# Optimization experiments

Hardware: AMD Instinct MI355X
Metric: run time of the kernel (lower is better)

The kernel has to match this reference:

```python
import jax, jax.numpy as jnp
import numpy as np

EPS = 1e-5

def _offset_conv(x, w, b):
    # 3x3 conv, padding=1, producing 2*K*K offset channels (standard DeformConv2D v1)
    out = jax.lax.conv_general_dilated(x, w, (1, 1), ((1, 1), (1, 1)),
                                       dimension_numbers=('NCHW', 'OIHW', 'NCHW'))
    return out + b[None, :, None, None]

def _bilinear_gather(x, py, px):
    # x: [B,C,H,W]; py,px: [B,K2,H,W] float sample coords -> [B,C,K2,H,W]
    B, C, H, W = x.shape
    py = jnp.clip(py, 0.0, H - 1.0)
    px = jnp.clip(px, 0.0, W - 1.0)
    y0 = jnp.floor(py)
    x0 = jnp.floor(px)
    wy = py - y0
    wx = px - x0
    y0i = y0.astype(jnp.int32)
    x0i = x0.astype(jnp.int32)
    y1i = jnp.minimum(y0i + 1, H - 1)
    x1i = jnp.minimum(x0i + 1, W - 1)
    xf = x.reshape(B, C, H * W)
    K2, Ho, Wo = py.shape[1], py.shape[2], py.shape[3]
    def gather(yy, xx):
        idx = (yy * W + xx).reshape(B, 1, -1)  # broadcast over C
        return jnp.take_along_axis(xf, idx, axis=2).reshape(B, C, K2, Ho, Wo)
    v00 = gather(y0i, x0i)
    v01 = gather(y0i, x1i)
    v10 = gather(y1i, x0i)
    v11 = gather(y1i, x1i)
    wy = wy[:, None]
    wx = wx[:, None]
    return (v00 * (1 - wy) * (1 - wx) + v01 * (1 - wy) * wx
            + v10 * wy * (1 - wx) + v11 * wy * wx)

def _deform_dw(x, w_off, b_off, w_dw, k):
    # depthwise deformable conv, kernel k, padding k//2 (same spatial size)
    B, C, H, W = x.shape
    K2 = k * k
    off = _offset_conv(x, w_off, b_off)      # [B, 2*K2, H, W]
    dy, dx = off[:, :K2], off[:, K2:]
    r = (k - 1) // 2
    pn = jnp.arange(-r, r + 1, dtype=x.dtype)
    pn_y = jnp.repeat(pn, k)[None, :, None, None]  # [1,K2,1,1]
    pn_x = jnp.tile(pn, k)[None, :, None, None]
    gy = jnp.arange(H, dtype=x.dtype)[None, None, :, None]
    gx = jnp.arange(W, dtype=x.dtype)[None, None, None, :]
    py = gy + pn_y + dy
    px = gx + pn_x + dx
    samp = _bilinear_gather(x, py, px)        # [B,C,K2,H,W]
    return jnp.einsum('bckhw,ck->bchw', samp, w_dw.reshape(C, K2))

def _bn_relu(x, g, b, m, v):
    inv = g / jnp.sqrt(v + EPS)
    return jax.nn.relu(x * inv[None, :, None, None] + (b - m * inv)[None, :, None, None])

def setup_inputs() -> dict:
    key = jax.random.key(0)
    B, C, H, W, O = 4, 96, 64, 64, 192
    ks = jax.random.split(key, 32)
    d = {'x': jax.random.normal(ks[0], (B, C, H, W), jnp.float32)}
    i = 1
    for k in (3, 5, 7):
        K2 = k * k
        d[f'w_off{k}'] = 0.01 * jax.random.normal(ks[i], (2 * K2, C, 3, 3), jnp.float32); i += 1
        d[f'b_off{k}'] = jnp.zeros((2 * K2,), jnp.float32)
        d[f'w_dw{k}'] = jax.random.normal(ks[i], (C, k, k), jnp.float32) / k; i += 1
        d[f'g{k}'] = jnp.ones((C,), jnp.float32)
        d[f'be{k}'] = jnp.zeros((C,), jnp.float32)
        d[f'm{k}'] = 0.1 * jax.random.normal(ks[i], (C,), jnp.float32); i += 1
        d[f'v{k}'] = jax.random.uniform(ks[i], (C,), jnp.float32, 0.5, 1.5); i += 1
    d['w_pw'] = jax.random.normal(ks[i], (O, 3 * C), jnp.float32) / np.sqrt(3 * C).astype(np.float32); i += 1
    d['gp'] = jnp.ones((O,), jnp.float32)
    d['bp'] = jnp.zeros((O,), jnp.float32)
    d['mp'] = 0.1 * jax.random.normal(ks[i], (O,), jnp.float32); i += 1
    d['vp'] = jax.random.uniform(ks[i], (O,), jnp.float32, 0.5, 1.5)
    return d

def reference(x, w_off3, b_off3, w_dw3, g3, be3, m3, v3,
              w_off5, b_off5, w_dw5, g5, be5, m5, v5,
              w_off7, b_off7, w_dw7, g7, be7, m7, v7,
              w_pw, gp, bp, mp, vp):
    x1 = _bn_relu(_deform_dw(x, w_off3, b_off3, w_dw3, 3), g3, be3, m3, v3)
    x2 = _bn_relu(_deform_dw(x, w_off5, b_off5, w_dw5, 5), g5, be5, m5, v5)
    x3 = _bn_relu(_deform_dw(x, w_off7, b_off7, w_dw7, 7), g7, be7, m7, v7)
    xc = jnp.concatenate([x1, x2, x3], axis=1)  # [B, 3C, H, W]
    out = jnp.einsum('bchw,oc->bohw', xc, w_pw)  # 1x1 conv
    return _bn_relu(out, gp, bp, mp, vp)
```

## Files before the change

kernel.cpp:

```cpp
#include <hip/hip_runtime.h>
#include <hip/hip_fp16.h>
#include <math.h>

typedef unsigned short u16;
typedef _Float16 f16x8 __attribute__((ext_vector_type(8)));
typedef float f32x4 __attribute__((ext_vector_type(4)));

#define HWp 4096
#define Cc 96
#define Bb 4
#define Oo 192
#define C3 288

#define OFF_WDWT  0
#define OFF_BCAT  14112
#define OFF_SBR   14304
#define OFF_HBR   14592
#define OFF_SPW   14880
#define OFF_HPW   15072
#define FP32_END  15264
#define BF_XTPAD  0
#define BF_WOF    1672704
#define BF_WPW    1838592

__device__ __forceinline__ u16 f2h(float f) { return __half_as_ushort(__float2half(f)); }
__device__ __forceinline__ unsigned h2u(__half2 h) { union { __half2 h; unsigned u; } t; t.h = h; return t.u; }
__device__ __forceinline__ __half2 u2h(unsigned u) { union { __half2 h; unsigned u; } t; t.u = u; return t.h; }

#define PREP_N (165888 + 55296 + 14112 + 192 + 288 + 288 + 192 + 192 + 24960)
#define PREP_BLK ((PREP_N + 255) / 256)

__global__ __launch_bounds__(256) void prep_kernel(
    const float* __restrict__ x,
    const float* __restrict__ w3, const float* __restrict__ b3, const float* __restrict__ dw3,
    const float* __restrict__ g3, const float* __restrict__ be3, const float* __restrict__ m3, const float* __restrict__ v3,
    const float* __restrict__ w5, const float* __restrict__ b5, const float* __restrict__ dw5,
    const float* __restrict__ g5, const float* __restrict__ be5, const float* __restrict__ m5, const float* __restrict__ v5,
    const float* __restrict__ w7, const float* __restrict__ b7, const float* __restrict__ dw7,
    const float* __restrict__ g7, const float* __restrict__ be7, const float* __restrict__ m7, const float* __restrict__ v7,
    const float* __restrict__ wpw,
    const float* __restrict__ gp, const float* __restrict__ bp, const float* __restrict__ mp, const float* __restrict__ vp,
    float* __restrict__ ws)
{
    __shared__ u16 sT[64 * 104];
    u16* bf = (u16*)(ws + FP32_END);
    const int tid = threadIdx.x;

    if (blockIdx.x < 256) {
        const int b = blockIdx.x >> 6, h = blockIdx.x & 63;
        const float* xb = x + (((size_t)b * Cc) << 12) + (h << 6);
#pragma unroll
        for (int it = 0; it < 24; ++it) {
            int j = tid + it * 256;
            int c = j >> 6, p = j & 63;
            sT[p * 104 + c] = f2h(xb[((size_t)c << 12) + p]);
        }
        __syncthreads();
        u16* dst = bf + BF_XTPAD + ((size_t)(b * 66 + h + 1) * 66 + 1) * 96;
#pragma unroll
        for (int it = 0; it < 6; ++it) {
            int j = tid + it * 256;
            int pos = j / 24, c4 = j % 24;
            const u16* s = &sT[pos * 104 + c4 * 4];
            *(uint2*)(dst + pos * 96 + c4 * 4) = make_uint2(
                (unsigned)s[0] | ((unsigned)s[1] << 16),
                (unsigned)s[2] | ((unsigned)s[3] << 16));
        }
        return;
    }

    int i = (blockIdx.x - 256) * 256 + tid;
    if (i < 165888) {
        int f = i / 13824, r = i % 13824;
        int s = r >> 9, l = r & 511;
        int lane = l >> 3, j = l & 7;
        int o = f * 16 + (lane & 15);
        int k = s * 32 + (lane >> 4) * 8 + j;
        int tap = k / 96, c = k % 96;
        float v = 0.f;
        if (o < 18)       v = w3[o * 864 + c * 9 + tap];
        else if (o < 68)  v = w5[(o - 18) * 864 + c * 9 + tap];
        else if (o < 166) v = w7[(o - 68) * 864 + c * 9 + tap];
        bf[BF_WOF + i] = f2h(v);
        return;
    }
    int j = i - 165888;
    if (j < 55296) {
        int f = j / 4608, r = j % 4608;
        int s = r >> 9, l = r & 511;
        int lane = l >> 3, jj = l & 7;
        int o = f * 16 + (lane & 15);
        int k = s * 32 + (lane >> 4) * 8 + jj;
        bf[BF_WPW + j] = f2h(wpw[o * C3 + k]);
        return;
    }
    j -= 55296;
    if (j < 14112) {
        int ksel = j / 4704, rem = j % 4704;
        int t = rem / 96, c = rem % 96;
        int K2 = (ksel == 0) ? 9 : (ksel == 1) ? 25 : 49;
        const float* dw = (ksel == 0) ? dw3 : (ksel == 1) ? dw5 : dw7;
        ws[OFF_WDWT + j] = (t < K2) ? dw[c * K2 + t] : 0.f;
        return;
    }
    j -= 14112;
    if (j < 192) {
        float v = 0.f;
        if (j < 18)       v = b3[j];
        else if (j < 68)  v = b5[j - 18];
        else if (j < 166) v = b7[j - 68];
        ws[OFF_BCAT + j] = v;
        return;
    }
    j -= 192;
    if (j < C3) {
        int ks = j / Cc, c = j % Cc;
        const float* g = (ks == 0) ? g3 : (ks == 1) ? g5 : g7;
        const float* v = (ks == 0) ? v3 : (ks == 1) ? v5 : v7;
        ws[OFF_SBR + j] = g[c] / sqrtf(v[c] + 1e-5f);
        return;
    }
    j -= C3;
    if (j < C3) {
        int ks = j / Cc, c = j % Cc;
        const float* g = (ks == 0) ? g3 : (ks == 1) ? g5 : g7;
        const float* v = (ks == 0) ? v3 : (ks == 1) ? v5 : v7;
        const float* be = (ks == 0) ? be3 : (ks == 1) ? be5 : be7;
        const float* m = (ks == 0) ? m3 : (ks == 1) ? m5 : m7;
        float inv = g[c] / sqrtf(v[c] + 1e-5f);
        ws[OFF_HBR + j] = be[c] - m[c] * inv;
        return;
    }
    j -= C3;
    if (j < Oo) { ws[OFF_SPW + j] = gp[j] / sqrtf(vp[j] + 1e-5f); return; }
    j -= Oo;
    if (j < Oo) {
        float inv = gp[j] / sqrtf(vp[j] + 1e-5f);
        ws[OFF_HPW + j] = bp[j] - mp[j] * inv;
        return;
    }
    j -= Oo;
    if (j < 24960) {
        int c4 = j % 24, rem = j / 24;
        int cell = rem % 260, bb = rem / 260;
        int row, col;
        if (cell < 66)       { row = 0;  col = cell; }
        else if (cell < 132) { row = 65; col = cell - 66; }
        else if (cell < 196) { row = cell - 132 + 1; col = 0; }
        else                 { row = cell - 196 + 1; col = 65; }
        u16* dst = bf + BF_XTPAD + ((size_t)(bb * 66 + row) * 66 + col) * 96 + c4 * 4;
        *(uint2*)dst = make_uint2(0u, 0u);
        return;
    }
}

__global__ __launch_bounds__(256, 4) void mega_kernel(
    const float* __restrict__ ws, float* __restrict__ out)
{
    __shared__ uint4 regA[1328];
    __shared__ float regB[3072];
    u16* sX = (u16*)regA;
    uint4* sWI = regA;
    float* soff = regB;
    u16* ytile = (u16*)regB;

    const u16* bf = (const u16*)(ws + FP32_END);
    const u16* xp = bf + BF_XTPAD;
    const int tid = threadIdx.x;
    const int lane = tid & 63, wid = tid >> 6;
    const int lane15 = lane & 15, quad = lane >> 4;

    const int bx = blockIdx.x;
    const int xcd = bx & 7;
    const int b = xcd >> 1;
    const int tile = ((bx >> 3) << 1) + (xcd & 1);
    const int p0 = tile * 16;
    const int h = p0 >> 6;
    const int w0 = p0 & 63;

    {
        const u16* src = xp + ((size_t)(b * 66 + h) * 66 + w0) * 96;
        for (int j = tid; j < 1296; j += 256) {
            int r = j / 432;
            int rem = j % 432;
            int col = rem / 24, c4 = rem % 24;
            uint2 v = *(const uint2*)(src + ((size_t)(r * 66 + col)) * 96 + c4 * 4);
            *(uint2*)(&sX[(r * 18 + col) * 104 + c4 * 4]) = v;
        }
    }
    __syncthreads();

    {
        const u16* wof = bf + BF_WOF;
        f32x4 acc[3];
#pragma unroll
        for (int ff = 0; ff < 3; ++ff) acc[ff] = (f32x4){0.f, 0.f, 0.f, 0.f};
#pragma unroll
        for (int tap = 0; tap < 9; ++tap) {
            const int ky2 = tap / 3, kx2 = tap % 3;
            const u16* brow = &sX[(ky2 * 18 + kx2 + lane15) * 104 + quad * 8];
#pragma unroll
            for (int cc = 0; cc < 3; ++cc) {
                f16x8 bb = *(const f16x8*)(brow + cc * 32);
                const int s = tap * 3 + cc;
#pragma unroll
                for (int ff = 0; ff < 3; ++ff) {
                    const int f = wid * 3 + ff;
                    f16x8 a = *(const f16x8*)(wof + ((size_t)(f * 27 + s) * 64 + lane) * 8);
                    acc[ff] = __builtin_amdgcn_mfma_f32_16x16x32_f16(a, bb, acc[ff], 0, 0, 0);
                }
            }
        }
        const float* bcat = ws + OFF_BCAT;
#pragma unroll
        for (int ff = 0; ff < 3; ++ff) {
#pragma unroll
            for (int r = 0; r < 4; ++r) {
                int co = (wid * 3 + ff) * 16 + quad * 4 + r;
                soff[co * 16 + lane15] = acc[ff][r] + bcat[co];
            }
        }
    }
    __syncthreads();

    for (int i = tid; i < 1328; i += 256) {
        int gt = i >> 4, q = i & 15;
        int K, K2, R, tb, t;
        if (gt < 9)       { K = 3; K2 = 9;  R = 1; tb = 0;  t = gt; }
        else if (gt < 34) { K = 5; K2 = 25; R = 2; tb = 18; t = gt - 9; }
        else              { K = 7; K2 = 49; R = 3; tb = 68; t = gt - 34; }
        int ky = t / K - R, kx = t % K - R;
        float dy = soff[(tb + t) * 16 + q];
        float dx = soff[(tb + K2 + t) * 16 + q];
        float py = fminf(fmaxf((float)(h + ky) + dy, 0.f), 63.f);
        float px = fminf(fmaxf((float)(w0 + q + kx) + dx, 0.f), 63.f);
        float fy = floorf(py), fx = floorf(px);
        int y0 = (int)fy, x0 = (int)fx;
        float wy = py - fy, wx = px - fx;
        int y1 = min(y0 + 1, 63), x1 = min(x0 + 1, 63);
        float w11 = wy * wx;
        float w10 = wy - w11;
        float w01 = wx - w11;
        float w00 = 1.f - wy - wx + w11;
        unsigned wA = h2u(__floats2half2_rn(w00, w01));
        unsigned wB = h2u(__floats2half2_rn(w10, w11));
        unsigned o00 = (unsigned)((y0 + 1) * 66 + (x0 + 1)) * 192u;
        unsigned d01 = (unsigned)(x1 - x0) * 192u;
        unsigned d10 = (unsigned)(y1 - y0) * 12672u;
        sWI[i] = make_uint4(wA, wB, o00, d01 | (d10 << 16));
    }
    __syncthreads();

    if (tid < 192) {
        const int c8 = tid % 12;
        const int q  = tid / 12;
        const int c = c8 * 8;
        const u16* xh = xp + (size_t)b * 66 * 66 * 96;
        const char* xcb = (const char*)xh + c * 2;

#pragma unroll
        for (int seg = 0; seg < 3; ++seg) {
            const int g0 = (seg == 0) ? 0 : (seg == 1) ? 9 : 34;
            const int g1 = (seg == 0) ? 9 : (seg == 1) ? 34 : 83;
            const float* wdT = ws + OFF_WDWT + seg * 4704 + c;
            float acc[8];
#pragma unroll
            for (int k = 0; k < 8; ++k) acc[k] = 0.f;

            for (int gt = g0; gt < g1; ++gt) {
                const uint4 e = sWI[(gt << 4) + q];
                const __half2 wAh = u2h(e.x), wBh = u2h(e.y);
                const __half2 w00b = __low2half2(wAh), w01b = __high2half2(wAh);
                const __half2 w10b = __low2half2(wBh), w11b = __high2half2(wBh);
                const unsigned d01 = e.w & 0xffffu, d10 = e.w >> 16;
                const uint4 u00 = *(const uint4*)(xcb + e.z);
                const uint4 u01 = *(const uint4*)(xcb + e.z + d01);
                const uint4 u10 = *(const uint4*)(xcb + e.z + d10);
                const uint4 u11 = *(const uint4*)(xcb + e.z + d10 + d01);
                const float4 wda = *(const float4*)(wdT + (gt - g0) * 96);
                const float4 wdb = *(const float4*)(wdT + (gt - g0) * 96 + 4);
                const unsigned a00[4] = {u00.x, u00.y, u00.z, u00.w};
                const unsigned a01[4] = {u01.x, u01.y, u01.z, u01.w};
                const unsigned a10[4] = {u10.x, u10.y, u10.z, u10.w};
                const unsigned a11[4] = {u11.x, u11.y, u11.z, u11.w};
                const float wd[8] = {wda.x, wda.y, wda.z, wda.w, wdb.x, wdb.y, wdb.z, wdb.w};
#pragma unroll
                for (int d = 0; d < 4; ++d) {
                    __half2 v = __hmul2(w00b, u2h(a00[d]));
                    v = __hfma2(w01b, u2h(a01[d]), v);
                    v = __hfma2(w10b, u2h(a10[d]), v);
                    v = __hfma2(w11b, u2h(a11[d]), v);
                    acc[2 * d]     = fmaf(wd[2 * d],     __low2float(v),  acc[2 * d]);
                    acc[2 * d + 1] = fmaf(wd[2 * d + 1], __high2float(v), acc[2 * d + 1]);
                }
            }

            const int cb = seg * Cc + c;
            const float4 sa = *(const float4*)(ws + OFF_SBR + cb);
            const float4 sb = *(const float4*)(ws + OFF_SBR + cb + 4);
            const float4 ha = *(const float4*)(ws + OFF_HBR + cb);
            const float4 hb = *(const float4*)(ws + OFF_HBR + cb + 4);
            const float ss[8] = {sa.x, sa.y, sa.z, sa.w, sb.x, sb.y, sb.z, sb.w};
            const float hh8[8] = {ha.x, ha.y, ha.z, ha.w, hb.x, hb.y, hb.z, hb.w};
            unsigned rr[4];
#pragma unroll
            for (int d = 0; d < 4; ++d) {
                float lo = fmaxf(fmaf(acc[2 * d],     ss[2 * d],     hh8[2 * d]),     0.f);
                float hi = fmaxf(fmaf(acc[2 * d + 1], ss[2 * d + 1], hh8[2 * d + 1]), 0.f);
                rr[d] = h2u(__floats2half2_rn(lo, hi));
            }
            *(uint4*)(ytile + q * 296 + cb) = make_uint4(rr[0], rr[1], rr[2], rr[3]);
        }
    }
    __syncthreads();

    {
        const u16* wpw = bf + BF_WPW;
        f32x4 acc[3];
#pragma unroll
        for (int ff = 0; ff < 3; ++ff) acc[ff] = (f32x4){0.f, 0.f, 0.f, 0.f};
        const u16* brow = &ytile[lane15 * 296 + quad * 8];
#pragma unroll
        for (int s = 0; s < 9; ++s) {
            f16x8 bb = *(const f16x8*)(brow + s * 32);
#pragma unroll
            for (int ff = 0; ff < 3; ++ff) {
                const int f = wid * 3 + ff;
                f16x8 a = *(const f16x8*)(wpw + ((size_t)(f * 9 + s) * 64 + lane) * 8);
                acc[ff] = __builtin_amdgcn_mfma_f32_16x16x32_f16(a, bb, acc[ff], 0, 0, 0);
            }
        }
        const float* spw = ws + OFF_SPW;
        const float* hpw = ws + OFF_HPW;
        const int p = p0 + lane15;
#pragma unroll
        for (int ff = 0; ff < 3; ++ff) {
#pragma unroll
            for (int r = 0; r < 4; ++r) {
                int o = (wid * 3 + ff) * 16 + quad * 4 + r;
                out[(((size_t)(b * Oo + o)) << 12) + p] =
                    fmaxf(fmaf(acc[ff][r], spw[o], hpw[o]), 0.f);
            }
        }
    }
}

extern "C" void kernel_launch(void* const* d_in, const int* in_sizes, int n_in,
                              void* d_out, int out_size, void* d_ws, size_t ws_size,
                              hipStream_t stream)
{
    const float* x     = (const float*)d_in[0];
    const float* w3    = (const float*)d_in[1];
    const float* b3    = (const float*)d_in[2];
    const float* dw3   = (const float*)d_in[3];
    const float* g3    = (const float*)d_in[4];
    const float* be3   = (const float*)d_in[5];
    const float* m3    = (const float*)d_in[6];
    const float* v3    = (const float*)d_in[7];
    const float* w5    = (const float*)d_in[8];
    const float* b5    = (const float*)d_in[9];
    const float* dw5   = (const float*)d_in[10];
    const float* g5    = (const float*)d_in[11];
    const float* be5   = (const float*)d_in[12];
    const float* m5    = (const float*)d_in[13];
    const float* v5    = (const float*)d_in[14];
    const float* w7    = (const float*)d_in[15];
    const float* b7    = (const float*)d_in[16];
    const float* dw7   = (const float*)d_in[17];
    const float* g7    = (const float*)d_in[18];
    const float* be7   = (const float*)d_in[19];
    const float* m7    = (const float*)d_in[20];
    const float* v7    = (const float*)d_in[21];
    const float* wpw   = (const float*)d_in[22];
    const float* gp    = (const float*)d_in[23];
    const float* bp    = (const float*)d_in[24];
    const float* mp    = (const float*)d_in[25];
    const float* vp    = (const float*)d_in[26];

    float* ws = (float*)d_ws;
    float* out = (float*)d_out;

    {
        prep_kernel<<<256 + PREP_BLK, 256, 0, stream>>>(
            x,
            w3, b3, dw3, g3, be3, m3, v3,
            w5, b5, dw5, g5, be5, m5, v5,
            w7, b7, dw7, g7, be7, m7, v7,
            wpw, gp, bp, mp, vp, ws);
    }
    {
        mega_kernel<<<1024, 256, 0, stream>>>(ws, out);
    }
}
```

Baseline: 176.7 us.

## Interleave 3x3/5x5/7x7 deformable gathers by row and store offsets as fp16

The deformable gather phase now fully unrolls all 83 taps, ordered by kernel row so the three branches' samples run interleaved, with three accumulator sets live at once. This is meant to improve cache locality between neighbouring taps of different kernel sizes and to give the scheduler more independent loads. Offset-conv outputs are also stored in shared memory as fp16 instead of fp32, shrinking that buffer. The cost is much higher register pressure and code size, and some loss of precision in the offsets.

```diff
diff --git a/kernel.cpp b/kernel.cpp
--- a/kernel.cpp
+++ b/kernel.cpp
@@ -24,6 +24,7 @@
 #define BF_WPW    1838592
 
 __device__ __forceinline__ u16 f2h(float f) { return __half_as_ushort(__float2half(f)); }
+__device__ __forceinline__ float h2f(u16 u) { union { __half h; u16 u; } t; t.u = u; return __half2float(t.h); }
 __device__ __forceinline__ unsigned h2u(__half2 h) { union { __half2 h; unsigned u; } t; t.h = h; return t.u; }
 __device__ __forceinline__ __half2 u2h(unsigned u) { union { __half2 h; unsigned u; } t; t.u = u; return t.h; }
 
@@ -154,15 +155,61 @@
     }
 }
 
+#define GATHER_TAP(SEG, T, GT) do {                                          \
+    const uint4 e = sWI[((GT) << 4) + q];                                    \
+    const __half2 wAh = u2h(e.x), wBh = u2h(e.y);                            \
+    const __half2 w00b = __low2half2(wAh), w01b = __high2half2(wAh);         \
+    const __half2 w10b = __low2half2(wBh), w11b = __high2half2(wBh);         \
+    const unsigned d01 = e.w & 0xffffu, d10 = e.w >> 16;                     \
+    const uint4 u00 = *(const uint4*)(xcb + e.z);                            \
+    const uint4 u01 = *(const uint4*)(xcb + e.z + d01);                      \
+    const uint4 u10 = *(const uint4*)(xcb + e.z + d10);                      \
+    const uint4 u11 = *(const uint4*)(xcb + e.z + d10 + d01);                \
+    const float4 wda = *(const float4*)(wdT##SEG + (T) * 96);                \
+    const float4 wdb = *(const float4*)(wdT##SEG + (T) * 96 + 4);            \
+    const unsigned a00[4] = {u00.x, u00.y, u00.z, u00.w};                    \
+    const unsigned a01[4] = {u01.x, u01.y, u01.z, u01.w};                    \
+    const unsigned a10[4] = {u10.x, u10.y, u10.z, u10.w};                    \
+    const unsigned a11[4] = {u11.x, u11.y, u11.z, u11.w};                    \
+    const float wd[8] = {wda.x, wda.y, wda.z, wda.w, wdb.x, wdb.y, wdb.z, wdb.w}; \
+    _Pragma("unroll")                                                        \
+    for (int d = 0; d < 4; ++d) {                                            \
+        __half2 v = __hmul2(w00b, u2h(a00[d]));                              \
+        v = __hfma2(w01b, u2h(a01[d]), v);                                   \
+        v = __hfma2(w10b, u2h(a10[d]), v);                                   \
+        v = __hfma2(w11b, u2h(a11[d]), v);                                   \
+        acc##SEG[2 * d]     = fmaf(wd[2 * d],     __low2float(v),  acc##SEG[2 * d]);     \
+        acc##SEG[2 * d + 1] = fmaf(wd[2 * d + 1], __high2float(v), acc##SEG[2 * d + 1]); \
+    }                                                                        \
+} while (0)
+
+#define SEG_EPI(SEG) do {                                                    \
+    const int cb = (SEG) * Cc + c;                                           \
+    const float4 sa = *(const float4*)(ws + OFF_SBR + cb);                   \
+    const float4 sb = *(const float4*)(ws + OFF_SBR + cb + 4);               \
+    const float4 ha = *(const float4*)(ws + OFF_HBR + cb);                   \
+    const float4 hb = *(const float4*)(ws + OFF_HBR + cb + 4);               \
+    const float ss[8] = {sa.x, sa.y, sa.z, sa.w, sb.x, sb.y, sb.z, sb.w};    \
+    const float hh8[8] = {ha.x, ha.y, ha.z, ha.w, hb.x, hb.y, hb.z, hb.w};   \
+    unsigned rr[4];                                                          \
+    _Pragma("unroll")                                                        \
+    for (int d = 0; d < 4; ++d) {                                            \
+        float lo = fmaxf(fmaf(acc##SEG[2 * d],     ss[2 * d],     hh8[2 * d]),     0.f); \
+        float hi = fmaxf(fmaf(acc##SEG[2 * d + 1], ss[2 * d + 1], hh8[2 * d + 1]), 0.f); \
+        rr[d] = h2u(__floats2half2_rn(lo, hi));                              \
+    }                                                                        \
+    *(uint4*)(ytile + q * 296 + cb) = make_uint4(rr[0], rr[1], rr[2], rr[3]); \
+} while (0)
+
 __global__ __launch_bounds__(256, 4) void mega_kernel(
     const float* __restrict__ ws, float* __restrict__ out)
 {
     __shared__ uint4 regA[1328];
-    __shared__ float regB[3072];
+    __shared__ u16  regB[4736];
     u16* sX = (u16*)regA;
     uint4* sWI = regA;
-    float* soff = regB;
-    u16* ytile = (u16*)regB;
+    u16* soff = regB;
+    u16* ytile = regB;
 
     const u16* bf = (const u16*)(ws + FP32_END);
     const u16* xp = bf + BF_XTPAD;
@@ -217,7 +264,7 @@
 #pragma unroll
             for (int r = 0; r < 4; ++r) {
                 int co = (wid * 3 + ff) * 16 + quad * 4 + r;
-                soff[co * 16 + lane15] = acc[ff][r] + bcat[co];
+                soff[co * 16 + lane15] = f2h(acc[ff][r] + bcat[co]);
             }
         }
     }
@@ -230,8 +277,8 @@
         else if (gt < 34) { K = 5; K2 = 25; R = 2; tb = 18; t = gt - 9; }
         else              { K = 7; K2 = 49; R = 3; tb = 68; t = gt - 34; }
         int ky = t / K - R, kx = t % K - R;
-        float dy = soff[(tb + t) * 16 + q];
-        float dx = soff[(tb + K2 + t) * 16 + q];
+        float dy = h2f(soff[(tb + t) * 16 + q]);
+        float dx = h2f(soff[(tb + K2 + t) * 16 + q]);
         float py = fminf(fmaxf((float)(h + ky) + dy, 0.f), 63.f);
         float px = fminf(fmaxf((float)(w0 + q + kx) + dx, 0.f), 63.f);
         float fy = floorf(py), fx = floorf(px);
@@ -257,60 +304,40 @@
         const int c = c8 * 8;
         const u16* xh = xp + (size_t)b * 66 * 66 * 96;
         const char* xcb = (const char*)xh + c * 2;
-
-#pragma unroll
-        for (int seg = 0; seg < 3; ++seg) {
-            const int g0 = (seg == 0) ? 0 : (seg == 1) ? 9 : 34;
-            const int g1 = (seg == 0) ? 9 : (seg == 1) ? 34 : 83;
-            const float* wdT = ws + OFF_WDWT + seg * 4704 + c;
-            float acc[8];
-#pragma unroll
-            for (int k = 0; k < 8; ++k) acc[k] = 0.f;
-
-            for (int gt = g0; gt < g1; ++gt) {
-                const uint4 e = sWI[(gt << 4) + q];
-                const __half2 wAh = u2h(e.x), wBh = u2h(e.y);
-                const __half2 w00b = __low2half2(wAh), w01b = __high2half2(wAh);
-                const __half2 w10b = __low2half2(wBh), w11b = __high2half2(wBh);
-                const unsigned d01 = e.w & 0xffffu, d10 = e.w >> 16;
-                const uint4 u00 = *(const uint4*)(xcb + e.z);
-                const uint4 u01 = *(const uint4*)(xcb + e.z + d01);
-                const uint4 u10 = *(const uint4*)(xcb + e.z + d10);
-                const uint4 u11 = *(const uint4*)(xcb + e.z + d10 + d01);
-                const float4 wda = *(const float4*)(wdT + (gt - g0) * 96);
-                const float4 wdb = *(const float4*)(wdT + (gt - g0) * 96 + 4);
-                const unsigned a00[4] = {u00.x, u00.y, u00.z, u00.w};
-                const unsigned a01[4] = {u01.x, u01.y, u01.z, u01.w};
-                const unsigned a10[4] = {u10.x, u10.y, u10.z, u10.w};
-                const unsigned a11[4] = {u11.x, u11.y, u11.z, u11.w};
-                const float wd[8] = {wda.x, wda.y, wda.z, wda.w, wdb.x, wdb.y, wdb.z, wdb.w};
-#pragma unroll
-                for (int d = 0; d < 4; ++d) {
-                    __half2 v = __hmul2(w00b, u2h(a00[d]));
-                    v = __hfma2(w01b, u2h(a01[d]), v);
-                    v = __hfma2(w10b, u2h(a10[d]), v);
-                    v = __hfma2(w11b, u2h(a11[d]), v);
-                    acc[2 * d]     = fmaf(wd[2 * d],     __low2float(v),  acc[2 * d]);
-                    acc[2 * d + 1] = fmaf(wd[2 * d + 1], __high2float(v), acc[2 * d + 1]);
+        const float* wdT0 = ws + OFF_WDWT + 0 * 4704 + c;
+        const float* wdT1 = ws + OFF_WDWT + 1 * 4704 + c;
+        const float* wdT2 = ws + OFF_WDWT + 2 * 4704 + c;
+
+        float acc0[8], acc1[8], acc2[8];
+#pragma unroll
+        for (int k = 0; k < 8; ++k) { acc0[k] = 0.f; acc1[k] = 0.f; acc2[k] = 0.f; }
+
+#pragma unroll
+        for (int ky = -3; ky <= 3; ++ky) {
+            if (ky >= -1 && ky <= 1) {
+#pragma unroll
+                for (int kx = -1; kx <= 1; ++kx) {
+                    const int t = (ky + 1) * 3 + (kx + 1);
+                    GATHER_TAP(0, t, t);
                 }
             }
-
-            const int cb = seg * Cc + c;
-            const float4 sa = *(const float4*)(ws + OFF_SBR + cb);
-            const float4 sb = *(const float4*)(ws + OFF_SBR + cb + 4);
-            const float4 ha = *(const float4*)(ws + OFF_HBR + cb);
-            const float4 hb = *(const float4*)(ws + OFF_HBR + cb + 4);
-            const float ss[8] = {sa.x, sa.y, sa.z, sa.w, sb.x, sb.y, sb.z, sb.w};
-            const float hh8[8] = {ha.x, ha.y, ha.z, ha.w, hb.x, hb.y, hb.z, hb.w};
-            unsigned rr[4];
-#pragma unroll
-            for (int d = 0; d < 4; ++d) {
-                float lo = fmaxf(fmaf(acc[2 * d],     ss[2 * d],     hh8[2 * d]),     0.f);
-                float hi = fmaxf(fmaf(acc[2 * d + 1], ss[2 * d + 1], hh8[2 * d + 1]), 0.f);
-                rr[d] = h2u(__floats2half2_rn(lo, hi));
-            }
-            *(uint4*)(ytile + q * 296 + cb) = make_uint4(rr[0], rr[1], rr[2], rr[3]);
-        }
+            if (ky >= -2 && ky <= 2) {
+#pragma unroll
+                for (int kx = -2; kx <= 2; ++kx) {
+                    const int t = (ky + 2) * 5 + (kx + 2);
+                    GATHER_TAP(1, t, 9 + t);
+                }
+            }
+#pragma unroll
+            for (int kx = -3; kx <= 3; ++kx) {
+                const int t = (ky + 3) * 7 + (kx + 3);
+                GATHER_TAP(2, t, 34 + t);
+            }
+        }
+
+        SEG_EPI(0);
+        SEG_EPI(1);
+        SEG_EPI(2);
     }
     __syncthreads();
 
```

Measured after the change: 177.3 us. No clear change (+0.3%).

## Stage local input window in LDS for deformable bilinear gathers

Applied to the files above, without the earlier changes.

Each block now loads a 9x24 pixel window of the padded fp16 input around its tile into shared memory. Bilinear corner fetches whose sample point falls inside that window read from LDS, and only out-of-window samples fall back to global memory, signalled by a flag bit. Offsets are stored as fp16 to shrink the offset buffer. The larger LDS footprint forces launch bounds down from 4 to 2 blocks per CU, which lowers occupancy and adds a divergent branch in the gather loop.

```diff
diff --git a/kernel.cpp b/kernel.cpp
--- a/kernel.cpp
+++ b/kernel.cpp
@@ -24,6 +24,7 @@
 #define BF_WPW    1838592
 
 __device__ __forceinline__ u16 f2h(float f) { return __half_as_ushort(__float2half(f)); }
+__device__ __forceinline__ float h2f(u16 u) { union { __half h; u16 u; } t; t.u = u; return __half2float(t.h); }
 __device__ __forceinline__ unsigned h2u(__half2 h) { union { __half2 h; unsigned u; } t; t.h = h; return t.u; }
 __device__ __forceinline__ __half2 u2h(unsigned u) { union { __half2 h; unsigned u; } t; t.u = u; return t.h; }
 
@@ -154,15 +155,16 @@
     }
 }
 
-__global__ __launch_bounds__(256, 4) void mega_kernel(
+__global__ __launch_bounds__(256, 2) void mega_kernel(
     const float* __restrict__ ws, float* __restrict__ out)
 {
     __shared__ uint4 regA[1328];
-    __shared__ float regB[3072];
+    __shared__ u16  regB[4736];
+    __shared__ __align__(16) u16 win[9 * 24 * 104];
     u16* sX = (u16*)regA;
     uint4* sWI = regA;
-    float* soff = regB;
-    u16* ytile = (u16*)regB;
+    u16* soff = regB;
+    u16* ytile = regB;
 
     const u16* bf = (const u16*)(ws + FP32_END);
     const u16* xp = bf + BF_XTPAD;
@@ -178,11 +180,20 @@
     const int h = p0 >> 6;
     const int w0 = p0 & 63;
 
+    const int y_lo = min(max(h - 4, 0), 55);
+    const int x_lo = min(max(w0 - 4, 0), 40);
+
     {
+        const u16* srcw = xp + ((size_t)(b * 66 + y_lo + 1) * 66 + (x_lo + 1)) * 96;
+        for (int j = tid; j < 2592; j += 256) {
+            int r = j / 288, rem = j % 288;
+            int col = rem / 12, cg = rem % 12;
+            uint4 v = *(const uint4*)(srcw + ((size_t)(r * 66 + col)) * 96 + cg * 8);
+            *(uint4*)(&win[(r * 24 + col) * 104 + cg * 8]) = v;
+        }
         const u16* src = xp + ((size_t)(b * 66 + h) * 66 + w0) * 96;
         for (int j = tid; j < 1296; j += 256) {
-            int r = j / 432;
-            int rem = j % 432;
+            int r = j / 432, rem = j % 432;
             int col = rem / 24, c4 = rem % 24;
             uint2 v = *(const uint2*)(src + ((size_t)(r * 66 + col)) * 96 + c4 * 4);
             *(uint2*)(&sX[(r * 18 + col) * 104 + c4 * 4]) = v;
@@ -217,7 +228,7 @@
 #pragma unroll
             for (int r = 0; r < 4; ++r) {
                 int co = (wid * 3 + ff) * 16 + quad * 4 + r;
-                soff[co * 16 + lane15] = acc[ff][r] + bcat[co];
+                soff[co * 16 + lane15] = f2h(acc[ff][r] + bcat[co]);
             }
         }
     }
@@ -230,8 +241,8 @@
         else if (gt < 34) { K = 5; K2 = 25; R = 2; tb = 18; t = gt - 9; }
         else              { K = 7; K2 = 49; R = 3; tb = 68; t = gt - 34; }
         int ky = t / K - R, kx = t % K - R;
-        float dy = soff[(tb + t) * 16 + q];
-        float dx = soff[(tb + K2 + t) * 16 + q];
+        float dy = h2f(soff[(tb + t) * 16 + q]);
+        float dx = h2f(soff[(tb + K2 + t) * 16 + q]);
         float py = fminf(fmaxf((float)(h + ky) + dy, 0.f), 63.f);
         float px = fminf(fmaxf((float)(w0 + q + kx) + dx, 0.f), 63.f);
         float fy = floorf(py), fx = floorf(px);
@@ -244,39 +255,55 @@
         float w00 = 1.f - wy - wx + w11;
         unsigned wA = h2u(__floats2half2_rn(w00, w01));
         unsigned wB = h2u(__floats2half2_rn(w10, w11));
-        unsigned o00 = (unsigned)((y0 + 1) * 66 + (x0 + 1)) * 192u;
-        unsigned d01 = (unsigned)(x1 - x0) * 192u;
-        unsigned d10 = (unsigned)(y1 - y0) * 12672u;
-        sWI[i] = make_uint4(wA, wB, o00, d01 | (d10 << 16));
+        int y0r = y0 - y_lo, x0r = x0 - x_lo;
+        unsigned z, wpk;
+        if (y0r >= 0 && (y1 - y_lo) <= 8 && x0r >= 0 && (x1 - x_lo) <= 23) {
+            z   = (unsigned)((y0r * 24 + x0r) * 104);
+            wpk = (unsigned)((x1 - x0) * 104) | ((unsigned)((y1 - y0) * 2496) << 16);
+        } else {
+            z   = (unsigned)(((y0 + 1) * 66 + (x0 + 1)) * 96);
+            wpk = (unsigned)((x1 - x0) * 96) | ((unsigned)((y1 - y0) * 6336) << 16) | 0x80000000u;
+        }
+        sWI[i] = make_uint4(wA, wB, z, wpk);
     }
     __syncthreads();
 
     if (tid < 192) {
-        const int c8 = tid % 12;
+        const int cg = tid % 12;
         const int q  = tid / 12;
-        const int c = c8 * 8;
-        const u16* xh = xp + (size_t)b * 66 * 66 * 96;
-        const char* xcb = (const char*)xh + c * 2;
-
-#pragma unroll
+        const int c  = cg * 8;
+        const u16* xgc = xp + (size_t)b * 66 * 66 * 96 + c;
+        const u16* wlc = win + c;
+        const int segb[4] = {0, 9, 34, 83};
+
         for (int seg = 0; seg < 3; ++seg) {
-            const int g0 = (seg == 0) ? 0 : (seg == 1) ? 9 : 34;
-            const int g1 = (seg == 0) ? 9 : (seg == 1) ? 34 : 83;
             const float* wdT = ws + OFF_WDWT + seg * 4704 + c;
             float acc[8];
 #pragma unroll
             for (int k = 0; k < 8; ++k) acc[k] = 0.f;
+            const int g0 = segb[seg], g1 = segb[seg + 1];
 
             for (int gt = g0; gt < g1; ++gt) {
                 const uint4 e = sWI[(gt << 4) + q];
+                const unsigned d01 = e.w & 0xffffu;
+                const unsigned d10 = (e.w >> 16) & 0x7fffu;
+                uint4 u00, u01, u10, u11;
+                if (e.w & 0x80000000u) {
+                    const u16* p = xgc + e.z;
+                    u00 = *(const uint4*)p;
+                    u01 = *(const uint4*)(p + d01);
+                    u10 = *(const uint4*)(p + d10);
+                    u11 = *(const uint4*)(p + d10 + d01);
+                } else {
+                    const u16* p = wlc + e.z;
+                    u00 = *(const uint4*)p;
+                    u01 = *(const uint4*)(p + d01);
+                    u10 = *(const uint4*)(p + d10);
+                    u11 = *(const uint4*)(p + d10 + d01);
+                }
                 const __half2 wAh = u2h(e.x), wBh = u2h(e.y);
                 const __half2 w00b = __low2half2(wAh), w01b = __high2half2(wAh);
                 const __half2 w10b = __low2half2(wBh), w11b = __high2half2(wBh);
-                const unsigned d01 = e.w & 0xffffu, d10 = e.w >> 16;
-                const uint4 u00 = *(const uint4*)(xcb + e.z);
-                const uint4 u01 = *(const uint4*)(xcb + e.z + d01);
-                const uint4 u10 = *(const uint4*)(xcb + e.z + d10);
-                const uint4 u11 = *(const uint4*)(xcb + e.z + d10 + d01);
                 const float4 wda = *(const float4*)(wdT + (gt - g0) * 96);
                 const float4 wdb = *(const float4*)(wdT + (gt - g0) * 96 + 4);
                 const unsigned a00[4] = {u00.x, u00.y, u00.z, u00.w};
```

Result: slower. 201.7 us (+14.1%).
